# Kernel optimization log

Measured on AMD Instinct MI355X. Metric: run time of the kernel, lower is better.

## Reference

```python
import jax, jax.numpy as jnp
import numpy as np

B, F, Q, CHUNK = 2, 8192, 4096, 512
NUM_VERTS = 6000


def _safe_div(n, d):
    return n / jnp.where(d == 0, 1.0, d)


def _bary(a, b, c, p):
    """Barycentric coords of the closest point on triangle (a,b,c) to p.
    All args broadcastable [..., 3]; returns [..., 3] (u, v, w) with
    closest = u*a + v*b + w*c. Ericson, Real-Time Collision Detection."""
    ab = b - a; ac = c - a; ap = p - a
    d1 = jnp.sum(ab * ap, -1); d2 = jnp.sum(ac * ap, -1)
    bp = p - b
    d3 = jnp.sum(ab * bp, -1); d4 = jnp.sum(ac * bp, -1)
    cp_ = p - c
    d5 = jnp.sum(ab * cp_, -1); d6 = jnp.sum(ac * cp_, -1)
    vc = d1 * d4 - d3 * d2
    vb = d5 * d2 - d1 * d6
    va = d3 * d6 - d5 * d4
    v_ab = _safe_div(d1, d1 - d3)
    w_ac = _safe_div(d2, d2 - d6)
    w_bc = _safe_div(d4 - d3, (d4 - d3) + (d5 - d6))
    inv = _safe_div(1.0, va + vb + vc)
    v_in = vb * inv; w_in = vc * inv
    zero = jnp.zeros_like(d1); one = jnp.ones_like(d1)
    conds = [(d1 <= 0) & (d2 <= 0),
             (d3 >= 0) & (d4 <= d3),
             (vc <= 0) & (d1 >= 0) & (d3 <= 0),
             (d6 >= 0) & (d5 <= d6),
             (vb <= 0) & (d2 >= 0) & (d6 <= 0),
             (va <= 0) & (d4 >= d3) & (d5 >= d6)]
    u = jnp.select(conds, [one, zero, 1 - v_ab, zero, 1 - w_ac, zero], 1 - v_in - w_in)
    v = jnp.select(conds, [zero, one, v_ab, zero, zero, 1 - w_bc], v_in)
    w = jnp.select(conds, [zero, zero, zero, one, w_ac, w_bc], w_in)
    return jnp.stack([u, v, w], -1)


def _closest_faces(triangles, points, chunk=CHUNK):
    """Exact closest-triangle index per query point (replaces BVH search).
    triangles [B,F,3,3], points [B,Q,3] -> int32 [B,Q]."""
    tri = jax.lax.stop_gradient(triangles)
    pts = jax.lax.stop_gradient(points)
    bsz, nq = pts.shape[0], pts.shape[1]
    a = tri[:, :, 0]; b = tri[:, :, 1]; c = tri[:, :, 2]  # [B,F,3]

    def one_chunk(p_chunk):  # [B,CH,3]
        pa = p_chunk[:, :, None, :]                       # [B,CH,1,3]
        bc = _bary(a[:, None], b[:, None], c[:, None], pa)  # [B,CH,F,3]
        cp = (bc[..., 0:1] * a[:, None] + bc[..., 1:2] * b[:, None]
              + bc[..., 2:3] * c[:, None])                # [B,CH,F,3]
        d2 = jnp.sum((cp - pa) ** 2, -1)                  # [B,CH,F]
        return jnp.argmin(d2, axis=-1)                    # [B,CH]

    chunks = jnp.moveaxis(pts.reshape(bsz, nq // chunk, chunk, 3), 1, 0)
    idx = jax.lax.map(one_chunk, chunks)                  # [NC,B,CH]
    return jnp.moveaxis(idx, 0, 1).reshape(bsz, nq)


def setup_inputs() -> dict:
    key = jax.random.key(0)
    k1, k2, k3, k4, k5 = jax.random.split(key, 5)
    return {
        'triangles': jax.random.normal(k1, (B, F, 3, 3), dtype=jnp.float32),
        'points': jax.random.normal(k2, (B, Q, 3), dtype=jnp.float32),
        'normals': jax.random.normal(k3, (B, F, 3, 3), dtype=jnp.float32),
        'cmaps': jax.random.normal(k4, (B, F, 3, 3), dtype=jnp.float32),
        'faces': jax.random.randint(k5, (B, F, 3), 0, NUM_VERTS, dtype=jnp.int32),
    }


def reference(triangles, points, normals, cmaps, faces):
    closest_faces = _closest_faces(triangles, points)     # [B,Q]
    idx = closest_faces[:, :, None, None]
    tri_g = jnp.take_along_axis(triangles, idx, axis=1)   # [B,Q,3,3]
    nrm_g = jnp.take_along_axis(normals, idx, axis=1)
    cmp_g = jnp.take_along_axis(cmaps, idx, axis=1)
    bcs = _bary(tri_g[:, :, 0], tri_g[:, :, 1], tri_g[:, :, 2], points)  # [B,Q,3]
    bcs = jnp.clip(bcs, 0.0, 1.0)
    closest_points = jnp.einsum('bqk,bqkd->bqd', bcs, tri_g)
    closest_normals = jnp.einsum('bqk,bqkd->bqd', bcs, nrm_g)
    closest_cmaps = jnp.einsum('bqk,bqkd->bqd', bcs, cmp_g)
    residual = closest_points - points
    closest_fids = jnp.take_along_axis(faces, closest_faces[:, :, None], axis=1)  # [B,Q,3]
    closest_idx = jnp.take_along_axis(
        closest_fids, jnp.argmax(bcs, -1)[:, :, None], axis=2)[..., 0]            # [B,Q]
    return residual, closest_normals, closest_cmaps, closest_idx
```

## Files before the change

kernel.cpp:

```cpp
#include <hip/hip_runtime.h>
#include <float.h>

#define B_   2
#define F_   8192
#define Q_   4096
#define NC   128
#define FC   (F_/NC)
#define PTS  256
#define PPT  4

typedef float f2 __attribute__((ext_vector_type(2)));
typedef float f4u __attribute__((ext_vector_type(4), aligned(4)));
typedef unsigned int uint;

__device__ __forceinline__ f2 clamp01(f2 x) {
    f2 z = {0.f, 0.f}, o = {1.f, 1.f};
    return __builtin_elementwise_min(__builtin_elementwise_max(x, z), o);
}

__device__ __forceinline__ void bary_uvw(
    float ax, float ay, float az,
    float bx, float by, float bz,
    float cx, float cy, float cz,
    float px, float py, float pz,
    float& u, float& v, float& w)
{
#pragma clang fp contract(off)
    float abx = bx - ax, aby = by - ay, abz = bz - az;
    float acx = cx - ax, acy = cy - ay, acz = cz - az;
    float apx = px - ax, apy = py - ay, apz = pz - az;
    float d1 = abx*apx + aby*apy + abz*apz;
    float d2 = acx*apx + acy*apy + acz*apz;
    float bpx = px - bx, bpy = py - by, bpz = pz - bz;
    float d3 = abx*bpx + aby*bpy + abz*bpz;
    float d4 = acx*bpx + acy*bpy + acz*bpz;
    float qx = px - cx, qy = py - cy, qz = pz - cz;
    float d5 = abx*qx + aby*qy + abz*qz;
    float d6 = acx*qx + acy*qy + acz*qz;
    float vc = d1*d4 - d3*d2;
    float vb = d5*d2 - d1*d6;
    float va = d3*d6 - d5*d4;

    bool c1 = (d1 <= 0.f) && (d2 <= 0.f);
    bool c2 = (d3 >= 0.f) && (d4 <= d3);
    bool c3 = (vc <= 0.f) && (d1 >= 0.f) && (d3 <= 0.f);
    bool c4 = (d6 >= 0.f) && (d5 <= d6);
    bool c5 = (vb <= 0.f) && (d2 >= 0.f) && (d6 <= 0.f);
    bool c6 = (va <= 0.f) && (d4 >= d3) && (d5 >= d6);

    bool e1 = c1;
    bool p1 = !c1;
    bool e2 = p1 && c2;
    bool p2 = p1 && !c2;
    bool e3 = p2 && c3;
    bool p3 = p2 && !c3;
    bool e4 = p3 && c4;
    bool p4 = p3 && !c4;
    bool e5 = p4 && c5;
    bool p5 = p4 && !c5;
    bool e6 = p5 && c6;

    float d43 = d4 - d3;
    float d56 = d5 - d6;
    float n  = e3 ? d1        : (e5 ? d2        : (e6 ? d43         : 1.f));
    float dd = e3 ? (d1 - d3) : (e5 ? (d2 - d6) : (e6 ? (d43 + d56) : (va + vb + vc)));
    dd = (dd == 0.f) ? 1.f : dd;
    float t = n / dd;

    float vi = vb * t;
    float wi = vc * t;
    u = e1 ? 1.f : (e2 ? 0.f : (e3 ? 1.f - t : (e4 ? 0.f : (e5 ? 1.f - t : (e6 ? 0.f     : 1.f - vi - wi)))));
    v = e1 ? 0.f : (e2 ? 1.f : (e3 ? t       : (e4 ? 0.f : (e5 ? 0.f     : (e6 ? 1.f - t : vi)))));
    w = e1 ? 0.f : (e2 ? 0.f : (e3 ? 0.f     : (e4 ? 1.f : (e5 ? t       : (e6 ? t       : wi)))));
}

__device__ __forceinline__ f2 pair_dist(
    f2 px, f2 py, f2 pz,
    float ax, float ay, float az,
    float abx, float aby, float abz,
    float acx, float acy, float acz,
    float daa, float dcc, float dac, float dbc, float kk,
    float rdaa, float rdcc, float rdbc, float rnn)
{
    f2 apx = px - ax, apy = py - ay, apz = pz - az;
    f2 d1  = abx*apx + aby*apy + abz*apz;
    f2 d2  = acx*apx + acy*apy + acz*apz;
    f2 app = apx*apx + apy*apy + apz*apz;

    f2 t1 = d1*dcc - d2*dac;
    f2 t2 = d2*daa - d1*dac;
    f2 t12n = 1.f - (t1 + t2)*rnn;
    f2 sgr  = (d1*t1 + d2*t2)*rnn;
    f2 ins  = __builtin_elementwise_min(__builtin_elementwise_min(t1, t2), t12n);

    f2 td1 = d1 + d1;
    f2 tab = clamp01(d1 * rdaa);
    f2 rab = tab*(td1 - tab*daa);
    f2 tac = clamp01(d2 * rdcc);
    f2 rac = tac*((d2 + d2) - tac*dcc);
    f2 d43 = (d2 - d1) + kk;
    f2 sbc = clamp01(d43 * rdbc);
    f2 rbc = (td1 - daa) + sbc*((d43 + d43) - sbc*dbc);
    f2 rmax = __builtin_elementwise_max(__builtin_elementwise_max(rab, rac), rbc);

    f2 red;
    red.x = (ins.x >= 0.f) ? sgr.x : rmax.x;
    red.y = (ins.y >= 0.f) ? sgr.y : rmax.y;
    f2 z = {0.f, 0.f};
    return __builtin_elementwise_max(app - red, z);
}

__global__ __launch_bounds__(PTS, 4) void scan_kernel(
    const float* __restrict__ tri, const float* __restrict__ pts,
    uint2* __restrict__ keys)
{
    __shared__ float4 S[FC * 6];
    const int tid = threadIdx.x;
    const int pb = blockIdx.x, cb = blockIdx.y, bb = blockIdx.z;

    if (tid < FC) {
        const float* g = tri + ((size_t)bb * F_ + (size_t)cb * FC + tid) * 9;
        float ax = g[0], ay = g[1], az = g[2];
        float bx = g[3], by = g[4], bz = g[5];
        float cx = g[6], cy = g[7], cz = g[8];
        float abx = bx - ax, aby = by - ay, abz = bz - az;
        float acx = cx - ax, acy = cy - ay, acz = cz - az;
        float daa = abx*abx + aby*aby + abz*abz;
        float dcc = acx*acx + acy*acy + acz*acz;
        float dac = abx*acx + aby*acy + abz*acz;
        float dbc = daa + dcc - 2.f*dac;
        float nn  = daa*dcc - dac*dac;
        S[tid*6 + 0] = make_float4(ax, ay, az, daa);
        S[tid*6 + 1] = make_float4(abx, aby, abz, dcc);
        S[tid*6 + 2] = make_float4(acx, acy, acz, dac);
        S[tid*6 + 3] = make_float4(1.f/daa, 1.f/dcc, 1.f/dbc, 1.f/nn);
        S[tid*6 + 4] = make_float4(bx, by, bz, 0.f);
        S[tid*6 + 5] = make_float4(cx, cy, cz, 0.f);
    }
    __syncthreads();

    const int q0 = pb * (PTS * PPT) + tid * PPT;
    const float* p0 = pts + ((size_t)bb * Q_ + q0) * 3;
    f4u l0 = *(const f4u*)(p0);
    f4u l1 = *(const f4u*)(p0 + 4);
    f4u l2 = *(const f4u*)(p0 + 8);
    f2 pxA = {l0.x, l0.w}, pyA = {l0.y, l1.x}, pzA = {l0.z, l1.y};
    f2 pxB = {l1.z, l2.y}, pyB = {l1.w, l2.z}, pzB = {l2.x, l2.w};

    uint k00 = 0xFFFFFFFFu, k01 = 0xFFFFFFFFu;
    uint k10 = 0xFFFFFFFFu, k11 = 0xFFFFFFFFu;
    uint k20 = 0xFFFFFFFFu, k21 = 0xFFFFFFFFu;
    uint k30 = 0xFFFFFFFFu, k31 = 0xFFFFFFFFu;
    #pragma unroll 2
    for (int fl = 0; fl < FC; ++fl) {
        float4 c0 = S[fl*6 + 0];
        float4 c1 = S[fl*6 + 1];
        float4 c2 = S[fl*6 + 2];
        float4 c3 = S[fl*6 + 3];
        float daa = c0.w, dcc = c1.w, dac = c2.w;
        float dbc = daa + dcc - 2.f*dac;
        float kk  = daa - dac;

        f2 dA = pair_dist(pxA, pyA, pzA, c0.x, c0.y, c0.z,
                          c1.x, c1.y, c1.z, c2.x, c2.y, c2.z,
                          daa, dcc, dac, dbc, kk, c3.x, c3.y, c3.z, c3.w);
        f2 dB = pair_dist(pxB, pyB, pzB, c0.x, c0.y, c0.z,
                          c1.x, c1.y, c1.z, c2.x, c2.y, c2.z,
                          daa, dcc, dac, dbc, kk, c3.x, c3.y, c3.z, c3.w);

        uint kA0 = (__float_as_uint(dA.x) & 0xFFFFFFC0u) | (uint)fl;
        uint kA1 = (__float_as_uint(dA.y) & 0xFFFFFFC0u) | (uint)fl;
        uint kB0 = (__float_as_uint(dB.x) & 0xFFFFFFC0u) | (uint)fl;
        uint kB1 = (__float_as_uint(dB.y) & 0xFFFFFFC0u) | (uint)fl;
        uint lo, hi;
        lo = min(k00, kA0); hi = max(k00, kA0); k00 = lo; k01 = min(k01, hi);
        lo = min(k10, kA1); hi = max(k10, kA1); k10 = lo; k11 = min(k11, hi);
        lo = min(k20, kB0); hi = max(k20, kB0); k20 = lo; k21 = min(k21, hi);
        lo = min(k30, kB1); hi = max(k30, kB1); k30 = lo; k31 = min(k31, hi);
    }

    float pxs[4] = {l0.x, l0.w, l1.z, l2.y};
    float pys[4] = {l0.y, l1.x, l1.w, l2.z};
    float pzs[4] = {l0.z, l1.y, l2.x, l2.w};
    uint kk0[4] = {k00, k10, k20, k30};
    uint kk1[4] = {k01, k11, k21, k31};

    #pragma unroll
    for (int p = 0; p < 4; ++p) {
        float px = pxs[p], py = pys[p], pz = pzs[p];
        float dbest = FLT_MAX; int fbest = 0x7FFFFFFF;
        #pragma unroll
        for (int j = 0; j < 2; ++j) {
            int lf = (int)((j == 0 ? kk0[p] : kk1[p]) & 63u);
            float4 ra = S[lf*6 + 0];
            float4 rb = S[lf*6 + 4];
            float4 rc = S[lf*6 + 5];
            float u, v, w;
            bary_uvw(ra.x, ra.y, ra.z, rb.x, rb.y, rb.z, rc.x, rc.y, rc.z,
                     px, py, pz, u, v, w);
            float d2v;
            {
#pragma clang fp contract(off)
                float cpx = u*ra.x + v*rb.x + w*rc.x;
                float cpy = u*ra.y + v*rb.y + w*rc.y;
                float cpz = u*ra.z + v*rb.z + w*rc.z;
                float dx = cpx - px, dy = cpy - py, dz = cpz - pz;
                d2v = dx*dx + dy*dy + dz*dz;
            }
            int face = cb * FC + lf;
            if (d2v < dbest || (d2v == dbest && face < fbest)) { dbest = d2v; fbest = face; }
        }
        keys[((size_t)bb * Q_ + q0 + p) * NC + cb] = make_uint2(__float_as_uint(dbest), (uint)fbest);
    }
}

__global__ __launch_bounds__(256) void finalize_kernel(
    const float* __restrict__ tri, const float* __restrict__ pts,
    const float* __restrict__ nrm, const float* __restrict__ cmp,
    const int* __restrict__ faces,
    const uint2* __restrict__ keys,
    float* __restrict__ out)
{
#pragma clang fp contract(off)
    const int lane = threadIdx.x & 63;
    const int t = blockIdx.x * 4 + (threadIdx.x >> 6);
    const int bb = t >> 12;

    uint4 K = ((const uint4*)keys)[(size_t)t * (NC/2) + lane];
    float dbest = __uint_as_float(K.x); int fbest = (int)K.y;
    float d1v   = __uint_as_float(K.z); int f1v   = (int)K.w;
    if (d1v < dbest || (d1v == dbest && f1v < fbest)) { dbest = d1v; fbest = f1v; }
    for (int off = 32; off > 0; off >>= 1) {
        float od = __shfl_down(dbest, off);
        int   of = __shfl_down(fbest, off);
        if (od < dbest || (od == dbest && of < fbest)) { dbest = od; fbest = of; }
    }
    if (lane != 0) return;

    const float* pp = pts + (size_t)t * 3;
    float px = pp[0], py = pp[1], pz = pp[2];

    const int bestf = fbest;
    const float* tg = tri + ((size_t)bb * F_ + bestf) * 9;
    const float* ng = nrm + ((size_t)bb * F_ + bestf) * 9;
    const float* cg = cmp + ((size_t)bb * F_ + bestf) * 9;
    f4u TA = *(const f4u*)(tg), TB = *(const f4u*)(tg + 4);
    float TC = tg[8];
    f4u NA = *(const f4u*)(ng), NB = *(const f4u*)(ng + 4);
    float NCs = ng[8];
    f4u CA = *(const f4u*)(cg), CB = *(const f4u*)(cg + 4);
    float CC = cg[8];

    float u, v, w;
    bary_uvw(TA.x, TA.y, TA.z, TA.w, TB.x, TB.y, TB.z, TB.w, TC,
             px, py, pz, u, v, w);
    u = fminf(fmaxf(u, 0.f), 1.f);
    v = fminf(fmaxf(v, 0.f), 1.f);
    w = fminf(fmaxf(w, 0.f), 1.f);

    float cpx = u * TA.x + v * TA.w + w * TB.z;
    float cpy = u * TA.y + v * TB.x + w * TB.w;
    float cpz = u * TA.z + v * TB.y + w * TC;
    float nx  = u * NA.x + v * NA.w + w * NB.z;
    float ny  = u * NA.y + v * NB.x + w * NB.w;
    float nz  = u * NA.z + v * NB.y + w * NCs;
    float mx  = u * CA.x + v * CA.w + w * CB.z;
    float my  = u * CA.y + v * CB.x + w * CB.w;
    float mz  = u * CA.z + v * CB.y + w * CC;

    const size_t S3 = (size_t)B_ * Q_ * 3;
    out[(size_t)t * 3 + 0] = cpx - px;
    out[(size_t)t * 3 + 1] = cpy - py;
    out[(size_t)t * 3 + 2] = cpz - pz;
    out[S3 + (size_t)t * 3 + 0] = nx;
    out[S3 + (size_t)t * 3 + 1] = ny;
    out[S3 + (size_t)t * 3 + 2] = nz;
    out[2 * S3 + (size_t)t * 3 + 0] = mx;
    out[2 * S3 + (size_t)t * 3 + 1] = my;
    out[2 * S3 + (size_t)t * 3 + 2] = mz;

    int k = 0; float mm = u;
    if (v > mm) { mm = v; k = 1; }
    if (w > mm) { k = 2; }
    out[3 * S3 + t] = (float)faces[((size_t)bb * F_ + bestf) * 3 + k];
}

extern "C" void kernel_launch(void* const* d_in, const int* in_sizes, int n_in,
                              void* d_out, int out_size, void* d_ws, size_t ws_size,
                              hipStream_t stream) {
    const float* tri   = (const float*)d_in[0];
    const float* pts   = (const float*)d_in[1];
    const float* nrm   = (const float*)d_in[2];
    const float* cmp   = (const float*)d_in[3];
    const int*   faces = (const int*)d_in[4];
    float* out = (float*)d_out;

    uint2* keys = (uint2*)d_ws;

    dim3 g1(Q_ / (PTS * PPT), NC, B_);
    scan_kernel<<<g1, PTS, 0, stream>>>(tri, pts, keys);
    finalize_kernel<<<(B_ * Q_) / 4, 256, 0, stream>>>(
        tri, pts, nrm, cmp, faces, keys, out);
}
```

Measured before the change: 141.5 us.

## Fuse scan and finalize via 64-bit atomicMin keys and last-block counter

Each scan block now packs its per-chunk best (distance, face) into a 64-bit key and merges it into a single per-query slot with atomicMin, instead of writing all 128 chunk candidates to workspace. A per-point-group counter, seeded by a memset to all-ones, lets the last-arriving chunk block run the finalize step: gather the triangle, normal and cmap data, compute the outputs and write them. This removes the second kernel launch and the large keys buffer round trip. In exchange it adds a memset, heavy 64-bit atomic traffic on few addresses, and a serialized tail done by the last block of each group. The shared-memory row stride also changes from 6 to 7 float4, which likely reduces bank conflicts.

```diff
diff --git a/kernel.cpp b/kernel.cpp
--- a/kernel.cpp
+++ b/kernel.cpp
@@ -8,10 +8,12 @@
 #define FC   (F_/NC)
 #define PTS  256
 #define PPT  4
+#define NGRP 8
 
 typedef float f2 __attribute__((ext_vector_type(2)));
 typedef float f4u __attribute__((ext_vector_type(4), aligned(4)));
 typedef unsigned int uint;
+typedef unsigned long long ull;
 
 __device__ __forceinline__ f2 clamp01(f2 x) {
     f2 z = {0.f, 0.f}, o = {1.f, 1.f};
@@ -110,11 +112,15 @@
     return __builtin_elementwise_max(app - red, z);
 }
 
-__global__ __launch_bounds__(PTS, 4) void scan_kernel(
+__global__ __launch_bounds__(PTS, 4) void fused_kernel(
     const float* __restrict__ tri, const float* __restrict__ pts,
-    uint2* __restrict__ keys)
+    const float* __restrict__ nrm, const float* __restrict__ cmp,
+    const int* __restrict__ faces,
+    ull* __restrict__ key64, uint* __restrict__ cnt,
+    float* __restrict__ out)
 {
-    __shared__ float4 S[FC * 6];
+    __shared__ float4 S[FC * 7];
+    __shared__ int s_last;
     const int tid = threadIdx.x;
     const int pb = blockIdx.x, cb = blockIdx.y, bb = blockIdx.z;
 
@@ -130,12 +136,12 @@
         float dac = abx*acx + aby*acy + abz*acz;
         float dbc = daa + dcc - 2.f*dac;
         float nn  = daa*dcc - dac*dac;
-        S[tid*6 + 0] = make_float4(ax, ay, az, daa);
-        S[tid*6 + 1] = make_float4(abx, aby, abz, dcc);
-        S[tid*6 + 2] = make_float4(acx, acy, acz, dac);
-        S[tid*6 + 3] = make_float4(1.f/daa, 1.f/dcc, 1.f/dbc, 1.f/nn);
-        S[tid*6 + 4] = make_float4(bx, by, bz, 0.f);
-        S[tid*6 + 5] = make_float4(cx, cy, cz, 0.f);
+        S[tid*7 + 0] = make_float4(ax, ay, az, daa);
+        S[tid*7 + 1] = make_float4(abx, aby, abz, dcc);
+        S[tid*7 + 2] = make_float4(acx, acy, acz, dac);
+        S[tid*7 + 3] = make_float4(1.f/daa, 1.f/dcc, 1.f/dbc, 1.f/nn);
+        S[tid*7 + 4] = make_float4(bx, by, bz, 0.f);
+        S[tid*7 + 5] = make_float4(cx, cy, cz, 0.f);
     }
     __syncthreads();
 
@@ -153,10 +159,10 @@
     uint k30 = 0xFFFFFFFFu, k31 = 0xFFFFFFFFu;
     #pragma unroll 2
     for (int fl = 0; fl < FC; ++fl) {
-        float4 c0 = S[fl*6 + 0];
-        float4 c1 = S[fl*6 + 1];
-        float4 c2 = S[fl*6 + 2];
-        float4 c3 = S[fl*6 + 3];
+        float4 c0 = S[fl*7 + 0];
+        float4 c1 = S[fl*7 + 1];
+        float4 c2 = S[fl*7 + 2];
+        float4 c3 = S[fl*7 + 3];
         float daa = c0.w, dcc = c1.w, dac = c2.w;
         float dbc = daa + dcc - 2.f*dac;
         float kk  = daa - dac;
@@ -192,9 +198,9 @@
         #pragma unroll
         for (int j = 0; j < 2; ++j) {
             int lf = (int)((j == 0 ? kk0[p] : kk1[p]) & 63u);
-            float4 ra = S[lf*6 + 0];
-            float4 rb = S[lf*6 + 4];
-            float4 rc = S[lf*6 + 5];
+            float4 ra = S[lf*7 + 0];
+            float4 rb = S[lf*7 + 4];
+            float4 rc = S[lf*7 + 5];
             float u, v, w;
             bary_uvw(ra.x, ra.y, ra.z, rb.x, rb.y, rb.z, rc.x, rc.y, rc.z,
                      px, py, pz, u, v, w);
@@ -210,79 +216,72 @@
             int face = cb * FC + lf;
             if (d2v < dbest || (d2v == dbest && face < fbest)) { dbest = d2v; fbest = face; }
         }
-        keys[((size_t)bb * Q_ + q0 + p) * NC + cb] = make_uint2(__float_as_uint(dbest), (uint)fbest);
-    }
-}
-
-__global__ __launch_bounds__(256) void finalize_kernel(
-    const float* __restrict__ tri, const float* __restrict__ pts,
-    const float* __restrict__ nrm, const float* __restrict__ cmp,
-    const int* __restrict__ faces,
-    const uint2* __restrict__ keys,
-    float* __restrict__ out)
-{
+        ull key = ((ull)__float_as_uint(dbest) << 32) | (uint)fbest;
+        atomicMin(&key64[(size_t)bb * Q_ + q0 + p], key);
+    }
+
+    __threadfence();
+    __syncthreads();
+    if (tid == 0) {
+        uint old = atomicAdd(&cnt[bb * (Q_ / (PTS * PPT)) + pb], 1u);
+        s_last = (old == (uint)(NC - 2)) ? 1 : 0;
+    }
+    __syncthreads();
+    if (!s_last) return;
+
+    #pragma unroll
+    for (int p = 0; p < 4; ++p) {
+        const int t = bb * Q_ + q0 + p;
+        float px = pxs[p], py = pys[p], pz = pzs[p];
+        ull kv = atomicAdd(&key64[t], 0ULL);
+        const int bestf = (int)(kv & 0xFFFFFFFFull);
+
+        const float* tg = tri + ((size_t)bb * F_ + bestf) * 9;
+        const float* ng = nrm + ((size_t)bb * F_ + bestf) * 9;
+        const float* cg = cmp + ((size_t)bb * F_ + bestf) * 9;
+        f4u TA = *(const f4u*)(tg), TB = *(const f4u*)(tg + 4);
+        float TC = tg[8];
+        f4u NA = *(const f4u*)(ng), NB = *(const f4u*)(ng + 4);
+        float NCs = ng[8];
+        f4u CA = *(const f4u*)(cg), CB = *(const f4u*)(cg + 4);
+        float CC = cg[8];
+
+        float u, v, w;
+        bary_uvw(TA.x, TA.y, TA.z, TA.w, TB.x, TB.y, TB.z, TB.w, TC,
+                 px, py, pz, u, v, w);
+        {
 #pragma clang fp contract(off)
-    const int lane = threadIdx.x & 63;
-    const int t = blockIdx.x * 4 + (threadIdx.x >> 6);
-    const int bb = t >> 12;
-
-    uint4 K = ((const uint4*)keys)[(size_t)t * (NC/2) + lane];
-    float dbest = __uint_as_float(K.x); int fbest = (int)K.y;
-    float d1v   = __uint_as_float(K.z); int f1v   = (int)K.w;
-    if (d1v < dbest || (d1v == dbest && f1v < fbest)) { dbest = d1v; fbest = f1v; }
-    for (int off = 32; off > 0; off >>= 1) {
-        float od = __shfl_down(dbest, off);
-        int   of = __shfl_down(fbest, off);
-        if (od < dbest || (od == dbest && of < fbest)) { dbest = od; fbest = of; }
-    }
-    if (lane != 0) return;
-
-    const float* pp = pts + (size_t)t * 3;
-    float px = pp[0], py = pp[1], pz = pp[2];
-
-    const int bestf = fbest;
-    const float* tg = tri + ((size_t)bb * F_ + bestf) * 9;
-    const float* ng = nrm + ((size_t)bb * F_ + bestf) * 9;
-    const float* cg = cmp + ((size_t)bb * F_ + bestf) * 9;
-    f4u TA = *(const f4u*)(tg), TB = *(const f4u*)(tg + 4);
-    float TC = tg[8];
-    f4u NA = *(const f4u*)(ng), NB = *(const f4u*)(ng + 4);
-    float NCs = ng[8];
-    f4u CA = *(const f4u*)(cg), CB = *(const f4u*)(cg + 4);
-    float CC = cg[8];
-
-    float u, v, w;
-    bary_uvw(TA.x, TA.y, TA.z, TA.w, TB.x, TB.y, TB.z, TB.w, TC,
-             px, py, pz, u, v, w);
-    u = fminf(fmaxf(u, 0.f), 1.f);
-    v = fminf(fmaxf(v, 0.f), 1.f);
-    w = fminf(fmaxf(w, 0.f), 1.f);
-
-    float cpx = u * TA.x + v * TA.w + w * TB.z;
-    float cpy = u * TA.y + v * TB.x + w * TB.w;
-    float cpz = u * TA.z + v * TB.y + w * TC;
-    float nx  = u * NA.x + v * NA.w + w * NB.z;
-    float ny  = u * NA.y + v * NB.x + w * NB.w;
-    float nz  = u * NA.z + v * NB.y + w * NCs;
-    float mx  = u * CA.x + v * CA.w + w * CB.z;
-    float my  = u * CA.y + v * CB.x + w * CB.w;
-    float mz  = u * CA.z + v * CB.y + w * CC;
-
-    const size_t S3 = (size_t)B_ * Q_ * 3;
-    out[(size_t)t * 3 + 0] = cpx - px;
-    out[(size_t)t * 3 + 1] = cpy - py;
-    out[(size_t)t * 3 + 2] = cpz - pz;
-    out[S3 + (size_t)t * 3 + 0] = nx;
-    out[S3 + (size_t)t * 3 + 1] = ny;
-    out[S3 + (size_t)t * 3 + 2] = nz;
-    out[2 * S3 + (size_t)t * 3 + 0] = mx;
-    out[2 * S3 + (size_t)t * 3 + 1] = my;
-    out[2 * S3 + (size_t)t * 3 + 2] = mz;
-
-    int k = 0; float mm = u;
-    if (v > mm) { mm = v; k = 1; }
-    if (w > mm) { k = 2; }
-    out[3 * S3 + t] = (float)faces[((size_t)bb * F_ + bestf) * 3 + k];
+            u = fminf(fmaxf(u, 0.f), 1.f);
+            v = fminf(fmaxf(v, 0.f), 1.f);
+            w = fminf(fmaxf(w, 0.f), 1.f);
+
+            float cpx = u * TA.x + v * TA.w + w * TB.z;
+            float cpy = u * TA.y + v * TB.x + w * TB.w;
+            float cpz = u * TA.z + v * TB.y + w * TC;
+            float nx  = u * NA.x + v * NA.w + w * NB.z;
+            float ny  = u * NA.y + v * NB.x + w * NB.w;
+            float nz  = u * NA.z + v * NB.y + w * NCs;
+            float mx  = u * CA.x + v * CA.w + w * CB.z;
+            float my  = u * CA.y + v * CB.x + w * CB.w;
+            float mz  = u * CA.z + v * CB.y + w * CC;
+
+            const size_t S3 = (size_t)B_ * Q_ * 3;
+            out[(size_t)t * 3 + 0] = cpx - px;
+            out[(size_t)t * 3 + 1] = cpy - py;
+            out[(size_t)t * 3 + 2] = cpz - pz;
+            out[S3 + (size_t)t * 3 + 0] = nx;
+            out[S3 + (size_t)t * 3 + 1] = ny;
+            out[S3 + (size_t)t * 3 + 2] = nz;
+            out[2 * S3 + (size_t)t * 3 + 0] = mx;
+            out[2 * S3 + (size_t)t * 3 + 1] = my;
+            out[2 * S3 + (size_t)t * 3 + 2] = mz;
+
+            int k = 0; float mm = u;
+            if (v > mm) { mm = v; k = 1; }
+            if (w > mm) { k = 2; }
+            out[3 * S3 + t] = (float)faces[((size_t)bb * F_ + bestf) * 3 + k];
+        }
+    }
 }
 
 extern "C" void kernel_launch(void* const* d_in, const int* in_sizes, int n_in,
@@ -295,10 +294,11 @@
     const int*   faces = (const int*)d_in[4];
     float* out = (float*)d_out;
 
-    uint2* keys = (uint2*)d_ws;
+    ull*  key64 = (ull*)d_ws;
+    uint* cnt   = (uint*)((char*)d_ws + (size_t)B_ * Q_ * 8);
+
+    hipMemsetAsync(d_ws, 0xFF, (size_t)B_ * Q_ * 8 + NGRP * 4, stream);
 
     dim3 g1(Q_ / (PTS * PPT), NC, B_);
-    scan_kernel<<<g1, PTS, 0, stream>>>(tri, pts, keys);
-    finalize_kernel<<<(B_ * Q_) / 4, 256, 0, stream>>>(
-        tri, pts, nrm, cmp, faces, keys, out);
-}
+    fused_kernel<<<g1, PTS, 0, stream>>>(tri, pts, nrm, cmp, faces, key64, cnt, out);
+}
```

Result: slower. 171.3 us (+21.0%).
